# Kernel tuning notes

Measured on AMD Instinct MI355X. Metric: run time of the kernel, lower is better.

Reference implementation:

```python
import jax, jax.numpy as jnp
import numpy as np

B, T = 64, 512
N_EMB, HIDDEN, VOCAB = 768, 256, 3072


def setup_inputs() -> dict:
    key = jax.random.key(0)
    ks = jax.random.split(key, 5)
    def xavier(k, shape):
        bound = float(np.sqrt(6.0 / (shape[0] + shape[1])))
        return jax.random.uniform(k, shape, jnp.float32, -bound, bound)
    return {
        "idx": jax.random.randint(ks[0], (B, T), 0, VOCAB),
        "emb_table": jax.random.normal(ks[1], (VOCAB, N_EMB), jnp.float32),
        "Wxh": xavier(ks[2], (N_EMB, HIDDEN)),
        "Whh": xavier(ks[3], (HIDDEN, HIDDEN)),
        "Wy": xavier(ks[4], (HIDDEN, VOCAB)),
        "By": jnp.zeros((VOCAB,), jnp.float32),
        "Bh": jnp.zeros((HIDDEN,), jnp.float32),
    }


def reference(idx, emb_table, Wxh, Whh, Wy, By, Bh):
    # embedded: [B, T, E] -> scan over time with hidden carry [B, H]
    embedded = emb_table[idx]                      # gather
    xWxh = jnp.einsum('bte,eh->tbh', embedded, Wxh)  # precompute input projection

    def step(hidden, x_t):
        hidden = jnp.tanh(x_t + hidden @ Whh + Bh)
        return hidden, None

    h0 = jnp.zeros((idx.shape[0], Whh.shape[0]), embedded.dtype)
    hidden, _ = jax.lax.scan(step, h0, xWxh)
    # return_sequences=False: only the last step's output is returned
    out = hidden @ Wy + By
    return out, hidden
```

## Files before the change

### kernel.cpp

```cpp
#include <hip/hip_runtime.h>
#include <hip/hip_bf16.h>

typedef _Float16 half8 __attribute__((ext_vector_type(8)));
typedef _Float16 half2_t __attribute__((ext_vector_type(2)));
typedef float f32x4 __attribute__((ext_vector_type(4)));

#define B_SZ 64
#define T_SZ 512
#define E_SZ 768
#define H_SZ 256
#define V_SZ 3072

#define WS_X     0u
#define WS_WT    16777216u
#define WS_WQ    17170432u
#define WS_H     17301504u

static __device__ __forceinline__ float fast_tanh(float x) {
  float e = __builtin_amdgcn_exp2f(x * 2.8853900817779268f);
  return 1.0f - 2.0f * __builtin_amdgcn_rcpf(1.0f + e);
}

static __device__ __forceinline__ float dot2(unsigned int h2, unsigned int w2, float c) {
  return __builtin_amdgcn_fdot2(__builtin_bit_cast(half2_t, h2),
                                __builtin_bit_cast(half2_t, w2), c, false);
}

__global__ __launch_bounds__(256) void k0_convert(
    const float* __restrict__ Wxh,
    const float* __restrict__ Whh,
    _Float16* __restrict__ Wt,
    unsigned int* __restrict__ Wq)
{
  int gid = blockIdx.x * 256 + threadIdx.x;
  if (gid < E_SZ * H_SZ) {
    int e = gid >> 8, h = gid & 255;
    Wt[h * E_SZ + e] = (_Float16)Wxh[gid];
  }
  if (gid < 128 * H_SZ) {
    int p = gid >> 8, c = gid & 255;
    half2_t pk;
    pk[0] = (_Float16)Whh[(size_t)(2 * p)     * H_SZ + c];
    pk[1] = (_Float16)Whh[(size_t)(2 * p + 1) * H_SZ + c];
    Wq[gid] = __builtin_bit_cast(unsigned int, pk);
  }
}

__global__ __launch_bounds__(256) void k1_xproj(
    const int* __restrict__ idx,
    const float* __restrict__ emb,
    const _Float16* __restrict__ Wt,
    _Float16* __restrict__ x)
{
  const int tid  = threadIdx.x;
  const int w    = tid >> 6;
  const int lane = tid & 63;
  const int m16  = lane & 15;
  const int quad = lane >> 4;
  const int r = blockIdx.x * 64 + w * 16 + m16;
  const int t = r >> 6;
  const int b = r & 63;
  const int erow = idx[b * T_SZ + t];
  const float* Arow = emb + (size_t)erow * E_SZ + quad * 8;

  __shared__ __align__(16) _Float16 bp[2][16 * 64 * 8];
  int n_[4], kb_[4];
#pragma unroll
  for (int pp = 0; pp < 4; ++pp) {
    int f = tid + 256 * pp;
    n_[pp]  = ((f >> 6) << 4) | (f & 15);
    kb_[pp] = (f >> 4) & 3;
  }
  uint4 stg[4];
#pragma unroll
  for (int pp = 0; pp < 4; ++pp)
    stg[pp] = *(const uint4*)(Wt + (size_t)n_[pp] * E_SZ + kb_[pp] * 8);
  f32x4 af0 = *(const f32x4*)(Arow);
  f32x4 af1 = *(const f32x4*)(Arow + 4);

  f32x4 acc[16];
#pragma unroll
  for (int n = 0; n < 16; ++n) { f32x4 z = {0.f, 0.f, 0.f, 0.f}; acc[n] = z; }

#pragma unroll
  for (int pp = 0; pp < 4; ++pp)
    *(uint4*)(bp[0] + (size_t)(tid + 256 * pp) * 8) = stg[pp];
  __syncthreads();

#pragma unroll 1
  for (int ki = 0; ki < 24; ++ki) {
    const _Float16* cur = bp[ki & 1];
    f32x4 af0n = af0, af1n = af1;
    if (ki < 23) {
#pragma unroll
      for (int pp = 0; pp < 4; ++pp)
        stg[pp] = *(const uint4*)(Wt + (size_t)n_[pp] * E_SZ + (ki + 1) * 32 + kb_[pp] * 8);
      af0n = *(const f32x4*)(Arow + (ki + 1) * 32);
      af1n = *(const f32x4*)(Arow + (ki + 1) * 32 + 4);
    }
    half8 a;
#pragma unroll
    for (int e = 0; e < 4; ++e) { a[e] = (_Float16)af0[e]; a[4 + e] = (_Float16)af1[e]; }
#pragma unroll
    for (int nt = 0; nt < 16; ++nt) {
      half8 bb = *(const half8*)(cur + (size_t)(nt * 64 + lane) * 8);
      acc[nt] = __builtin_amdgcn_mfma_f32_16x16x32_f16(a, bb, acc[nt], 0, 0, 0);
    }
    if (ki < 23) {
#pragma unroll
      for (int pp = 0; pp < 4; ++pp)
        *(uint4*)(bp[(ki + 1) & 1] + (size_t)(tid + 256 * pp) * 8) = stg[pp];
      __syncthreads();
    }
    af0 = af0n; af1 = af1n;
  }
  const int rbase = blockIdx.x * 64 + w * 16 + quad * 4;
#pragma unroll
  for (int nt = 0; nt < 16; ++nt) {
    const int col = nt * 16 + m16;
#pragma unroll
    for (int rg = 0; rg < 4; ++rg) {
      x[(size_t)(rbase + rg) * H_SZ + col] = (_Float16)acc[nt][rg];
    }
  }
}

__global__ __launch_bounds__(512, 2) void k2_rnn(
    const unsigned int* __restrict__ Wq,
    const _Float16* __restrict__ x,
    const float* __restrict__ Bh,
    float* __restrict__ hout,
    float* __restrict__ hidout)
{
  const int b   = blockIdx.x;
  const int tid = threadIdx.x;
  const int g   = tid >> 8;
  const int c   = tid & 255;
  __shared__ __align__(16) _Float16 hb[2][H_SZ];
  __shared__ float part[H_SZ];

  unsigned int wc[64];
#pragma unroll
  for (int i = 0; i < 64; ++i)
    wc[i] = Wq[(size_t)(g * 64 + i) * H_SZ + c];

  const float bhj = Bh[c];
  const _Float16* xp = x + b * H_SZ + c;
  _Float16 xA = xp[0];
  _Float16 xB = xp[(size_t)(B_SZ * H_SZ)];
  if (tid < H_SZ) hb[1][tid] = (_Float16)0.f;
  float hval = 0.f;
  __syncthreads();

#define K2_STEP(HR, HW, XREG)                                          \
  {                                                                    \
    const uint4* hq4 = ((const uint4*)(HR)) + g * 16;                  \
    float a0 = 0.f, a1 = 0.f, a2 = 0.f, a3 = 0.f;                      \
    _Pragma("unroll")                                                  \
    for (int kk = 0; kk < 16; ++kk) {                                  \
      uint4 hq = hq4[kk];                                              \
      a0 = dot2(hq.x, wc[4 * kk + 0], a0);                             \
      a1 = dot2(hq.y, wc[4 * kk + 1], a1);                             \
      a2 = dot2(hq.z, wc[4 * kk + 2], a2);                             \
      a3 = dot2(hq.w, wc[4 * kk + 3], a3);                             \
    }                                                                  \
    float psum = (a0 + a1) + (a2 + a3);                                \
    if (g) part[c] = psum;                                             \
    __syncthreads();                                                   \
    if (!g) {                                                          \
      float y = psum + part[c] + (float)(XREG) + bhj;                  \
      hval = fast_tanh(y);                                             \
      (HW)[c] = (_Float16)hval;                                        \
    }                                                                  \
    __syncthreads();                                                   \
  }

#pragma unroll 1
  for (int tt = 0; tt < 256; ++tt) {
    int ta = 2 * tt + 2; ta = ta > 511 ? 511 : ta;
    _Float16 xAc = xA;
    xA = xp[(size_t)ta * (B_SZ * H_SZ)];
    K2_STEP(hb[1], hb[0], xAc)
    int tb = 2 * tt + 3; tb = tb > 511 ? 511 : tb;
    _Float16 xBc = xB;
    xB = xp[(size_t)tb * (B_SZ * H_SZ)];
    K2_STEP(hb[0], hb[1], xBc)
  }
#undef K2_STEP
  if (!g) {
    hout[b * H_SZ + c] = hval;
    hidout[b * H_SZ + c] = hval;
  }
}

__global__ __launch_bounds__(256) void k3_out(
    const float* __restrict__ h,
    const float* __restrict__ Wy,
    const float* __restrict__ By,
    float* __restrict__ out)
{
  __shared__ float hs[H_SZ];
  const int c = blockIdx.x;
  const int b = blockIdx.y;
  const int v = c * 256 + threadIdx.x;
  hs[threadIdx.x] = h[b * H_SZ + threadIdx.x];
  __syncthreads();
  float acc = By[v];
#pragma unroll 8
  for (int jj = 0; jj < H_SZ; ++jj) {
    acc += hs[jj] * Wy[(size_t)jj * V_SZ + v];
  }
  out[(size_t)b * V_SZ + v] = acc;
}

extern "C" void kernel_launch(void* const* d_in, const int* in_sizes, int n_in,
                              void* d_out, int out_size, void* d_ws, size_t ws_size,
                              hipStream_t stream)
{
  const int*   idx = (const int*)d_in[0];
  const float* emb = (const float*)d_in[1];
  const float* Wxh = (const float*)d_in[2];
  const float* Whh = (const float*)d_in[3];
  const float* Wy  = (const float*)d_in[4];
  const float* By  = (const float*)d_in[5];
  const float* Bh  = (const float*)d_in[6];

  char* ws = (char*)d_ws;
  _Float16*     x    = (_Float16*)(ws + WS_X);
  _Float16*     Wt   = (_Float16*)(ws + WS_WT);
  unsigned int* Wq   = (unsigned int*)(ws + WS_WQ);
  float*        hbuf = (float*)(ws + WS_H);

  float* out    = (float*)d_out;
  float* hidout = out + (size_t)B_SZ * V_SZ;

  k0_convert<<<768, 256, 0, stream>>>(Wxh, Whh, Wt, Wq);
  k1_xproj  <<<512, 256, 0, stream>>>(idx, emb, Wt, x);
  k2_rnn    <<<64, 512, 0, stream>>>(Wq, x, Bh, hbuf, hidout);
  k3_out    <<<dim3(12, 64), 256, 0, stream>>>(hbuf, Wy, By, out);
}
```

Baseline: 443.7 us.

## Split RNN recurrence K-dimension across four thread groups per batch row

The recurrent kernel now uses 1024 threads per block instead of 512, so each output column's 256-long dot product is split into four 64-long partial sums instead of two. Partial sums go through a three-slot shared buffer and group 0 combines them. Hidden-state loads are hoisted ahead of the dot products, and empty asm barriers keep the halved weight slice pinned in registers. The aim is a shorter serial dependency chain in each timestep, at the cost of an extra shared-memory add per step and more warps taking part in each block barrier.

Result: no change. 442.0 us (-0.4%).

```diff
diff --git a/kernel.cpp b/kernel.cpp
--- a/kernel.cpp
+++ b/kernel.cpp
@@ -125,7 +125,7 @@
   }
 }
 
-__global__ __launch_bounds__(512, 2) void k2_rnn(
+__global__ __launch_bounds__(1024, 4) void k2_rnn(
     const unsigned int* __restrict__ Wq,
     const _Float16* __restrict__ x,
     const float* __restrict__ Bh,
@@ -137,12 +137,12 @@
   const int g   = tid >> 8;
   const int c   = tid & 255;
   __shared__ __align__(16) _Float16 hb[2][H_SZ];
-  __shared__ float part[H_SZ];
-
-  unsigned int wc[64];
-#pragma unroll
-  for (int i = 0; i < 64; ++i)
-    wc[i] = Wq[(size_t)(g * 64 + i) * H_SZ + c];
+  __shared__ float part[3][H_SZ];
+
+  unsigned int wc[32];
+#pragma unroll
+  for (int i = 0; i < 32; ++i)
+    wc[i] = Wq[(size_t)(g * 32 + i) * H_SZ + c];
 
   const float bhj = Bh[c];
   const _Float16* xp = x + b * H_SZ + c;
@@ -152,23 +152,26 @@
   float hval = 0.f;
   __syncthreads();
 
+#define DOT4(Q, KB) \
+  a0 = dot2(Q.x, wc[4 * (KB) + 0], a0); \
+  a1 = dot2(Q.y, wc[4 * (KB) + 1], a1); \
+  a2 = dot2(Q.z, wc[4 * (KB) + 2], a2); \
+  a3 = dot2(Q.w, wc[4 * (KB) + 3], a3);
+
 #define K2_STEP(HR, HW, XREG)                                          \
   {                                                                    \
-    const uint4* hq4 = ((const uint4*)(HR)) + g * 16;                  \
+    const uint4* hq4 = ((const uint4*)(HR)) + g * 8;                   \
+    uint4 q0 = hq4[0], q1 = hq4[1], q2 = hq4[2], q3 = hq4[3],          \
+          q4 = hq4[4], q5 = hq4[5], q6 = hq4[6], q7 = hq4[7];          \
     float a0 = 0.f, a1 = 0.f, a2 = 0.f, a3 = 0.f;                      \
-    _Pragma("unroll")                                                  \
-    for (int kk = 0; kk < 16; ++kk) {                                  \
-      uint4 hq = hq4[kk];                                              \
-      a0 = dot2(hq.x, wc[4 * kk + 0], a0);                             \
-      a1 = dot2(hq.y, wc[4 * kk + 1], a1);                             \
-      a2 = dot2(hq.z, wc[4 * kk + 2], a2);                             \
-      a3 = dot2(hq.w, wc[4 * kk + 3], a3);                             \
-    }                                                                  \
+    DOT4(q0, 0) DOT4(q1, 1) DOT4(q2, 2) DOT4(q3, 3)                    \
+    DOT4(q4, 4) DOT4(q5, 5) DOT4(q6, 6) DOT4(q7, 7)                    \
     float psum = (a0 + a1) + (a2 + a3);                                \
-    if (g) part[c] = psum;                                             \
+    if (g) part[g - 1][c] = psum;                                      \
     __syncthreads();                                                   \
     if (!g) {                                                          \
-      float y = psum + part[c] + (float)(XREG) + bhj;                  \
+      float y = psum + part[0][c] + part[1][c] + part[2][c]            \
+                + (float)(XREG) + bhj;                                 \
       hval = fast_tanh(y);                                             \
       (HW)[c] = (_Float16)hval;                                        \
     }                                                                  \
@@ -177,6 +180,14 @@
 
 #pragma unroll 1
   for (int tt = 0; tt < 256; ++tt) {
+    asm volatile("" : "+v"(wc[0]), "+v"(wc[1]), "+v"(wc[2]), "+v"(wc[3]),
+                      "+v"(wc[4]), "+v"(wc[5]), "+v"(wc[6]), "+v"(wc[7]));
+    asm volatile("" : "+v"(wc[8]), "+v"(wc[9]), "+v"(wc[10]), "+v"(wc[11]),
+                      "+v"(wc[12]), "+v"(wc[13]), "+v"(wc[14]), "+v"(wc[15]));
+    asm volatile("" : "+v"(wc[16]), "+v"(wc[17]), "+v"(wc[18]), "+v"(wc[19]),
+                      "+v"(wc[20]), "+v"(wc[21]), "+v"(wc[22]), "+v"(wc[23]));
+    asm volatile("" : "+v"(wc[24]), "+v"(wc[25]), "+v"(wc[26]), "+v"(wc[27]),
+                      "+v"(wc[28]), "+v"(wc[29]), "+v"(wc[30]), "+v"(wc[31]));
     int ta = 2 * tt + 2; ta = ta > 511 ? 511 : ta;
     _Float16 xAc = xA;
     xA = xp[(size_t)ta * (B_SZ * H_SZ)];
@@ -187,6 +198,7 @@
     K2_STEP(hb[0], hb[1], xBc)
   }
 #undef K2_STEP
+#undef DOT4
   if (!g) {
     hout[b * H_SZ + c] = hval;
     hidout[b * H_SZ + c] = hval;
@@ -236,6 +248,6 @@
 
   k0_convert<<<768, 256, 0, stream>>>(Wxh, Whh, Wt, Wq);
   k1_xproj  <<<512, 256, 0, stream>>>(idx, emb, Wt, x);
-  k2_rnn    <<<64, 512, 0, stream>>>(Wq, x, Bh, hbuf, hidout);
+  k2_rnn    <<<64, 1024, 0, stream>>>(Wq, x, Bh, hbuf, hidout);
   k3_out    <<<dim3(12, 64), 256, 0, stream>>>(hbuf, Wy, By, out);
 }
```
